# Performance work log

Measured on AMD Instinct MI355X. Metric: run time of the kernel, lower is better.

The kernel has to match this reference:

```python
import jax, jax.numpy as jnp
import numpy as np

ALPHA_POS, ALPHA_NEG, GAMMA, TAU = 1.0, 2.0, 2.0, 0.7
LAMBDA_CP, MU_ECE, N_BINS = 6.0, 5.0, 15
N = 16777216


def setup_inputs() -> dict:
    key = jax.random.key(0)
    k1, k2, k3 = jax.random.split(key, 3)
    p_hat = jax.random.uniform(k1, (N,), dtype=jnp.float32)
    u_hat = jax.random.uniform(k2, (N,), dtype=jnp.float32)
    targets = jax.random.randint(k3, (N,), 0, 2, dtype=jnp.int32)
    return {"p_hat": p_hat, "u_hat": u_hat, "targets": targets}


def _ece(probs, labels):
    # bin b covers (b/n_bins, (b+1)/n_bins]; single-pass histogram via segment_sum
    bins = jnp.clip(jnp.ceil(probs * N_BINS).astype(jnp.int32) - 1, 0, N_BINS - 1)
    sum_p = jax.ops.segment_sum(probs, bins, num_segments=N_BINS)
    sum_y = jax.ops.segment_sum(labels, bins, num_segments=N_BINS)
    # (|I_b|/N)*|mean_y - mean_p| == |sum_y - sum_p| / N ; empty bins contribute 0
    n = probs.shape[0]
    return jnp.sum(jnp.abs(sum_y - sum_p)) / n


def reference(p_hat, u_hat, targets):
    t = targets.astype(p_hat.dtype)
    pos = targets == 1
    pt = jnp.where(pos, p_hat, 1.0 - p_hat)
    alpha = jnp.where(pos, ALPHA_POS, ALPHA_NEG)
    focal = jnp.mean(-alpha * (1.0 - pt) ** GAMMA * jnp.log(pt + 1e-12))

    mask_ow = (~pos) & (p_hat > TAU)   # overconfident wrong
    mask_uc = pos & (p_hat < TAU)      # underconfident correct
    penalty = jnp.where(mask_ow, (1.0 - u_hat) ** 2,
                        jnp.where(mask_uc, u_hat ** 2, 0.0))
    cp_loss = jnp.mean(penalty)

    ece = _ece(p_hat, t)
    return focal + LAMBDA_CP * cp_loss + MU_ECE * ece
```

## Files before the change

kernel.cpp:

```cpp
#include <hip/hip_runtime.h>

#define NB 15
#define NV 17
#define BLOCK 256
#define BIGGRID 2048


__device__ __forceinline__ void process_elem(float pk, float uk, int tk,
                                             float& facc, float& cacc,
                                             float* bins)
{
    bool pos = (tk == 1);

    float pt  = pos ? pk : 1.0f - pk;
    float om  = 1.0f - pt;
    float l2  = __log2f(pt + 1e-12f);
    float f   = om * om * l2;
    float na  = pos ? -0.69314718055994531f : -1.38629436111989062f;
    facc = fmaf(f, na, facc);

    float thr = pos ? 0.7f : 0.3f;
    float s   = pos ? uk : 1.0f - uk;
    float s2  = s * s;
    float pen = (pt < thr) ? s2 : 0.0f;
    cacc += pen;

    int b = (int)ceilf(pk * 15.0f) - 1;
    b = min(max(b, 0), NB - 1);
    float v = (pos ? 1.0f : 0.0f) - pk;
    #pragma unroll
    for (int j = 0; j < NB; ++j)
        bins[j] += (b == j) ? v : 0.0f;
}

__global__ __launch_bounds__(BLOCK) void fcl_main(
    const float* __restrict__ p_hat,
    const float* __restrict__ u_hat,
    const int*   __restrict__ targets,
    float* __restrict__ partials,
    int n4, int n)
{
    float bins[NB];
    #pragma unroll
    for (int j = 0; j < NB; ++j) bins[j] = 0.0f;
    float facc = 0.0f, cacc = 0.0f;

    const float4* __restrict__ p4 = (const float4*)p_hat;
    const float4* __restrict__ u4 = (const float4*)u_hat;
    const int4*   __restrict__ t4 = (const int4*)targets;

    const int stride = gridDim.x * blockDim.x;
    int i = blockIdx.x * blockDim.x + threadIdx.x;

    for (; i + stride < n4; i += 2 * stride) {
        float4 p0 = p4[i];          float4 p1 = p4[i + stride];
        float4 u0 = u4[i];          float4 u1 = u4[i + stride];
        int4   t0 = t4[i];          int4   t1 = t4[i + stride];
        #pragma unroll
        for (int k = 0; k < 4; ++k)
            process_elem((&p0.x)[k], (&u0.x)[k], (&t0.x)[k], facc, cacc, bins);
        #pragma unroll
        for (int k = 0; k < 4; ++k)
            process_elem((&p1.x)[k], (&u1.x)[k], (&t1.x)[k], facc, cacc, bins);
    }
    if (i < n4) {
        float4 p0 = p4[i]; float4 u0 = u4[i]; int4 t0 = t4[i];
        #pragma unroll
        for (int k = 0; k < 4; ++k)
            process_elem((&p0.x)[k], (&u0.x)[k], (&t0.x)[k], facc, cacc, bins);
    }

    if (blockIdx.x == 0 && threadIdx.x == 0) {
        for (int j = n4 * 4; j < n; ++j)
            process_elem(p_hat[j], u_hat[j], targets[j], facc, cacc, bins);
    }

    float vals[NV];
    vals[0] = facc; vals[1] = cacc;
    #pragma unroll
    for (int j = 0; j < NB; ++j) vals[2 + j] = bins[j];

    #pragma unroll
    for (int off = 32; off > 0; off >>= 1) {
        #pragma unroll
        for (int j = 0; j < NV; ++j)
            vals[j] += __shfl_down(vals[j], off, 64);
    }

    __shared__ float lds[BLOCK / 64][NV];
    const int wave = threadIdx.x >> 6;
    const int lane = threadIdx.x & 63;
    if (lane == 0) {
        #pragma unroll
        for (int j = 0; j < NV; ++j) lds[wave][j] = vals[j];
    }
    __syncthreads();

    if (threadIdx.x < NV) {
        float s = 0.0f;
        #pragma unroll
        for (int w = 0; w < BLOCK / 64; ++w) s += lds[w][threadIdx.x];
        partials[threadIdx.x * gridDim.x + blockIdx.x] = s;
    }
}

__global__ __launch_bounds__(1024) void fcl_final(
    const float* __restrict__ partials,
    float* __restrict__ out, float inv_n, int grid)
{
    const int t = threadIdx.x;
    float v[NV];
    #pragma unroll
    for (int j = 0; j < NV; ++j) {
        float s = 0.0f;
        for (int g = t; g < grid; g += 1024)
            s += partials[j * grid + g];
        v[j] = s;
    }

    #pragma unroll
    for (int off = 32; off > 0; off >>= 1) {
        #pragma unroll
        for (int j = 0; j < NV; ++j)
            v[j] += __shfl_down(v[j], off, 64);
    }

    __shared__ float lds[16][NV];
    const int wave = t >> 6;
    const int lane = t & 63;
    if (lane == 0) {
        #pragma unroll
        for (int j = 0; j < NV; ++j) lds[wave][j] = v[j];
    }
    __syncthreads();

    if (t == 0) {
        float s[NV];
        #pragma unroll
        for (int j = 0; j < NV; ++j) s[j] = 0.0f;
        for (int w = 0; w < 16; ++w)
            #pragma unroll
            for (int j = 0; j < NV; ++j) s[j] += lds[w][j];
        float e = 0.0f;
        #pragma unroll
        for (int b = 0; b < NB; ++b) e += fabsf(s[2 + b]);
        out[0] = (s[0] + 6.0f * s[1] + 5.0f * e) * inv_n;
    }
}

extern "C" void kernel_launch(void* const* d_in, const int* in_sizes, int n_in,
                              void* d_out, int out_size, void* d_ws, size_t ws_size,
                              hipStream_t stream) {
    const float* p = (const float*)d_in[0];
    const float* u = (const float*)d_in[1];
    const int*   t = (const int*)d_in[2];
    float* out = (float*)d_out;
    float* ws  = (float*)d_ws;

    const int n  = in_sizes[0];
    const int n4 = n / 4;

    const int grid = (ws_size >= (size_t)(NV * BIGGRID) * sizeof(float)) ? BIGGRID : 1024;

    fcl_main<<<grid, BLOCK, 0, stream>>>(p, u, t, ws, n4, n);
    fcl_final<<<1, 1024, 0, stream>>>(ws, out, 1.0f / (float)n, grid);
}
```

Baseline: 218.6 us.

## Fuse final reduction into main kernel via last-block atomic counter and nontemporal loads

Folds the separate single-block final reduction into the main kernel: each block writes its partials, fences, and bumps an atomic counter, and the last block to arrive reduces all partials and writes the output. A tiny init kernel resets the counter before each run. Input loads also switch to nontemporal vector loads to reduce cache pollution on streaming data. The final reduction now runs with 256 threads instead of 1024, and a launch is still spent on the counter reset.

```diff
diff --git a/kernel.cpp b/kernel.cpp
--- a/kernel.cpp
+++ b/kernel.cpp
@@ -5,6 +5,9 @@
 #define BLOCK 256
 #define BIGGRID 2048
 
+
+typedef float f32x4 __attribute__((ext_vector_type(4)));
+typedef int   i32x4 __attribute__((ext_vector_type(4)));
 
 __device__ __forceinline__ void process_elem(float pk, float uk, int tk,
                                              float& facc, float& cacc,
@@ -21,8 +24,7 @@
 
     float thr = pos ? 0.7f : 0.3f;
     float s   = pos ? uk : 1.0f - uk;
-    float s2  = s * s;
-    float pen = (pt < thr) ? s2 : 0.0f;
+    float pen = (pt < thr) ? s * s : 0.0f;
     cacc += pen;
 
     int b = (int)ceilf(pk * 15.0f) - 1;
@@ -33,41 +35,53 @@
         bins[j] += (b == j) ? v : 0.0f;
 }
 
-__global__ __launch_bounds__(BLOCK) void fcl_main(
+__global__ void fcl_init(unsigned int* __restrict__ counter)
+{
+    *counter = 0u;
+}
+
+__global__ __launch_bounds__(BLOCK) void fcl_fused(
     const float* __restrict__ p_hat,
     const float* __restrict__ u_hat,
     const int*   __restrict__ targets,
     float* __restrict__ partials,
-    int n4, int n)
+    unsigned int* __restrict__ counter,
+    float* __restrict__ out,
+    float inv_n, int n4, int n, int grid)
 {
     float bins[NB];
     #pragma unroll
     for (int j = 0; j < NB; ++j) bins[j] = 0.0f;
     float facc = 0.0f, cacc = 0.0f;
 
-    const float4* __restrict__ p4 = (const float4*)p_hat;
-    const float4* __restrict__ u4 = (const float4*)u_hat;
-    const int4*   __restrict__ t4 = (const int4*)targets;
+    const f32x4* __restrict__ p4 = (const f32x4*)p_hat;
+    const f32x4* __restrict__ u4 = (const f32x4*)u_hat;
+    const i32x4* __restrict__ t4 = (const i32x4*)targets;
 
-    const int stride = gridDim.x * blockDim.x;
-    int i = blockIdx.x * blockDim.x + threadIdx.x;
+    const int stride = grid * BLOCK;
+    int i = blockIdx.x * BLOCK + threadIdx.x;
 
     for (; i + stride < n4; i += 2 * stride) {
-        float4 p0 = p4[i];          float4 p1 = p4[i + stride];
-        float4 u0 = u4[i];          float4 u1 = u4[i + stride];
-        int4   t0 = t4[i];          int4   t1 = t4[i + stride];
+        f32x4 p0 = __builtin_nontemporal_load(p4 + i);
+        f32x4 p1 = __builtin_nontemporal_load(p4 + i + stride);
+        f32x4 u0 = __builtin_nontemporal_load(u4 + i);
+        f32x4 u1 = __builtin_nontemporal_load(u4 + i + stride);
+        i32x4 t0 = __builtin_nontemporal_load(t4 + i);
+        i32x4 t1 = __builtin_nontemporal_load(t4 + i + stride);
         #pragma unroll
         for (int k = 0; k < 4; ++k)
-            process_elem((&p0.x)[k], (&u0.x)[k], (&t0.x)[k], facc, cacc, bins);
+            process_elem(p0[k], u0[k], t0[k], facc, cacc, bins);
         #pragma unroll
         for (int k = 0; k < 4; ++k)
-            process_elem((&p1.x)[k], (&u1.x)[k], (&t1.x)[k], facc, cacc, bins);
+            process_elem(p1[k], u1[k], t1[k], facc, cacc, bins);
     }
     if (i < n4) {
-        float4 p0 = p4[i]; float4 u0 = u4[i]; int4 t0 = t4[i];
+        f32x4 p0 = __builtin_nontemporal_load(p4 + i);
+        f32x4 u0 = __builtin_nontemporal_load(u4 + i);
+        i32x4 t0 = __builtin_nontemporal_load(t4 + i);
         #pragma unroll
         for (int k = 0; k < 4; ++k)
-            process_elem((&p0.x)[k], (&u0.x)[k], (&t0.x)[k], facc, cacc, bins);
+            process_elem(p0[k], u0[k], t0[k], facc, cacc, bins);
     }
 
     if (blockIdx.x == 0 && threadIdx.x == 0) {
@@ -100,20 +114,22 @@
         float s = 0.0f;
         #pragma unroll
         for (int w = 0; w < BLOCK / 64; ++w) s += lds[w][threadIdx.x];
-        partials[threadIdx.x * gridDim.x + blockIdx.x] = s;
+        partials[threadIdx.x * grid + blockIdx.x] = s;
     }
-}
 
-__global__ __launch_bounds__(1024) void fcl_final(
-    const float* __restrict__ partials,
-    float* __restrict__ out, float inv_n, int grid)
-{
-    const int t = threadIdx.x;
+    __threadfence();
+    __shared__ unsigned int amLast;
+    if (threadIdx.x == 0)
+        amLast = (atomicAdd(counter, 1u) == (unsigned int)(grid - 1)) ? 1u : 0u;
+    __syncthreads();
+    if (amLast == 0u) return;
+    __threadfence();
+
     float v[NV];
     #pragma unroll
     for (int j = 0; j < NV; ++j) {
         float s = 0.0f;
-        for (int g = t; g < grid; g += 1024)
+        for (int g = (int)threadIdx.x; g < grid; g += BLOCK)
             s += partials[j * grid + g];
         v[j] = s;
     }
@@ -125,20 +141,17 @@
             v[j] += __shfl_down(v[j], off, 64);
     }
 
-    __shared__ float lds[16][NV];
-    const int wave = t >> 6;
-    const int lane = t & 63;
     if (lane == 0) {
         #pragma unroll
         for (int j = 0; j < NV; ++j) lds[wave][j] = v[j];
     }
     __syncthreads();
 
-    if (t == 0) {
+    if (threadIdx.x == 0) {
         float s[NV];
         #pragma unroll
         for (int j = 0; j < NV; ++j) s[j] = 0.0f;
-        for (int w = 0; w < 16; ++w)
+        for (int w = 0; w < BLOCK / 64; ++w)
             #pragma unroll
             for (int j = 0; j < NV; ++j) s[j] += lds[w][j];
         float e = 0.0f;
@@ -160,8 +173,12 @@
     const int n  = in_sizes[0];
     const int n4 = n / 4;
 
-    const int grid = (ws_size >= (size_t)(NV * BIGGRID) * sizeof(float)) ? BIGGRID : 1024;
+    const int grid = (ws_size >= (size_t)(NV * BIGGRID + 1) * sizeof(float))
+                         ? BIGGRID : 1024;
+    float*        partials = ws;
+    unsigned int* counter  = (unsigned int*)(ws + (size_t)NV * grid);
 
-    fcl_main<<<grid, BLOCK, 0, stream>>>(p, u, t, ws, n4, n);
-    fcl_final<<<1, 1024, 0, stream>>>(ws, out, 1.0f / (float)n, grid);
+    fcl_init<<<1, 1, 0, stream>>>(counter);
+    fcl_fused<<<grid, BLOCK, 0, stream>>>(p, u, t, partials, counter, out,
+                                          1.0f / (float)n, n4, n, grid);
 }
```

After: 533.2 us. +143.9%, slower.
